# Performance work log

Hardware: AMD Instinct MI355X
Metric: run time of the kernel (lower is better)

Reference implementation:

```python
import jax, jax.numpy as jnp
import numpy as np

N_NODES = 100_000
N_EDGES = 1_600_000
IN_F = 256
HID = 256
OUT_F = 256
BN_EPS = 1e-5


def make_quaternion_mul(kernel):
    # kernel: [d, 4m] -> hamilton: [4d, 4m]
    dim = kernel.shape[1] // 4
    r, i, j, k = jnp.split(kernel, 4, axis=1)
    r2 = jnp.concatenate([r, -i, -j, -k], axis=0)
    i2 = jnp.concatenate([i, r, -k, j], axis=0)
    j2 = jnp.concatenate([j, k, r, -i], axis=0)
    k2 = jnp.concatenate([k, -j, i, r], axis=0)
    return jnp.concatenate([r2, i2, j2, k2], axis=1)


def setup_inputs() -> dict:
    key = jax.random.key(0)
    ks = jax.random.split(key, 6)
    x = jax.random.normal(ks[0], (N_NODES, IN_F), dtype=jnp.float32)
    rows = jax.random.randint(ks[1], (N_EDGES,), 0, N_NODES, dtype=jnp.int32)
    cols = jax.random.randint(ks[2], (N_EDGES,), 0, N_NODES, dtype=jnp.int32)
    edge_vals = jax.random.uniform(ks[3], (N_EDGES,), dtype=jnp.float32)
    stdv1 = np.sqrt(6.0 / (IN_F // 4 + HID))
    weight1 = jax.random.uniform(ks[4], (IN_F // 4, HID), dtype=jnp.float32,
                                 minval=-stdv1, maxval=stdv1)
    stdv2 = np.sqrt(6.0 / (HID // 4 + OUT_F))
    weight2 = jax.random.uniform(ks[5], (HID // 4, OUT_F), dtype=jnp.float32,
                                 minval=-stdv2, maxval=stdv2)
    gamma = jnp.ones((HID,), dtype=jnp.float32)
    beta = jnp.zeros((HID,), dtype=jnp.float32)
    return {"x": x, "rows": rows, "cols": cols, "edge_vals": edge_vals,
            "weight1": weight1, "weight2": weight2, "gamma": gamma, "beta": beta}


def reference(x, rows, cols, edge_vals, weight1, weight2, gamma, beta):
    hamilton1 = make_quaternion_mul(weight1)  # [IN_F, HID]
    hamilton2 = make_quaternion_mul(weight2)  # [HID, OUT_F]
    # spmm: new_x[r] = sum_e adj[r,c]*x[c] over edges (r=rows, c=cols)
    gathered = edge_vals[:, None] * x[cols]               # [E, IN_F]
    new_x = jax.ops.segment_sum(gathered, rows, num_segments=N_NODES)
    out1 = new_x @ hamilton1                              # [N, HID]
    # BatchNorm1d (training mode): biased batch stats over nodes
    mean = jnp.mean(out1, axis=0)
    var = jnp.mean(jnp.square(out1 - mean), axis=0)
    out1 = (out1 - mean) * jax.lax.rsqrt(var + BN_EPS) * gamma + beta
    out1 = jnp.tanh(out1)
    return out1 @ hamilton2                               # [N, OUT_F]
```

## Files before the change

kernel.cpp:

```cpp
#include <hip/hip_runtime.h>
#include <hip/hip_bf16.h>
#include <math.h>


#define FDIM 256
#define NREP 32
#define CH 2048

typedef __attribute__((ext_vector_type(8))) short bf16x8;
typedef __attribute__((ext_vector_type(4))) float f32x4;

static __device__ inline short f2bf(float x) {
    __hip_bfloat16 h = __float2bfloat16(x);
    return *reinterpret_cast<short*>(&h);
}
static __device__ inline float bf2f(unsigned short u) {
    union { unsigned int i; float f; } c;
    c.i = ((unsigned int)u) << 16;
    return c.f;
}
static __device__ inline float fast_tanh(float x) {
    float e = __expf(2.f * x);
    return 1.f - 2.f * __builtin_amdgcn_rcpf(e + 1.f);
}

static __device__ void build_hfrag(const float* __restrict__ w, ushort* __restrict__ hf,
                                   int t) {
    const int   comp_t[16] = {0,1,2,3,  1,0,3,2,  2,3,0,1,  3,2,1,0};
    const float sign_t[16] = {1,1,1,1, -1,1,1,-1, -1,-1,1,1, -1,1,-1,1};
    int f = t >> 6, lane = t & 63;
    int tile = f >> 3, kk = f & 7;
    int col = tile * 16 + (lane & 15);
    int b = col >> 6, q = col & 63;
    ushort o[8];
#pragma unroll
    for (int j = 0; j < 8; ++j) {
        int k = kk * 32 + ((lane >> 4) << 3) + j;
        int a = k >> 6, p = k & 63;
        int ab = a * 4 + b;
        float v = sign_t[ab] * w[p * 256 + comp_t[ab] * 64 + q];
        o[j] = (ushort)f2bf(v);
    }
    *(ushort4*)(hf + (size_t)t * 8)     = make_ushort4(o[0], o[1], o[2], o[3]);
    *(ushort4*)(hf + (size_t)t * 8 + 4) = make_ushort4(o[4], o[5], o[6], o[7]);
}

__global__ __launch_bounds__(256) void k_initp1(const float* __restrict__ w1,
                                                const float* __restrict__ w2,
                                                ushort* __restrict__ h1f,
                                                ushort* __restrict__ h2f,
                                                float* __restrict__ statsR,
                                                const int* __restrict__ rows,
                                                int* __restrict__ CM,
                                                int E, int nchunk, int NB) {
    int b = blockIdx.x;
    if (b < 32) {
        build_hfrag(w1, h1f, b * 256 + threadIdx.x);
        return;
    }
    if (b < 64) {
        build_hfrag(w2, h2f, (b - 32) * 256 + threadIdx.x);
        return;
    }
    if (b < 80) {
        int slot = (b - 64) * 256 + threadIdx.x;
        *(float4*)(statsR + slot * 4) = make_float4(0.f, 0.f, 0.f, 0.f);
        return;
    }
    __shared__ int lc[256];
    int t = threadIdx.x, c = b - 80;
    lc[t] = 0;
    __syncthreads();
#pragma unroll
    for (int i = 0; i < 8; ++i) {
        int e = c * CH + i * 256 + t;
        if (e < E) atomicAdd(&lc[rows[e] >> 9], 1);
    }
    __syncthreads();
    if (t < NB) CM[t * nchunk + c] = lc[t];
}

__global__ __launch_bounds__(256) void k_p2(const int* __restrict__ CM,
                                            int* __restrict__ PO,
                                            int* __restrict__ BT, int nchunk) {
    __shared__ int ts[256];
    int t = threadIdx.x, b = blockIdx.x;
    int base = b * nchunk;
    int lex[4], s = 0;
#pragma unroll
    for (int i = 0; i < 4; ++i) {
        int c = t * 4 + i;
        int v = (c < nchunk) ? CM[base + c] : 0;
        lex[i] = s;
        s += v;
    }
    ts[t] = s;
    __syncthreads();
    for (int off = 1; off < 256; off <<= 1) {
        int v = (t >= off) ? ts[t - off] : 0;
        __syncthreads();
        ts[t] += v;
        __syncthreads();
    }
    int excl = ts[t] - s;
#pragma unroll
    for (int i = 0; i < 4; ++i) {
        int c = t * 4 + i;
        if (c < nchunk) PO[base + c] = excl + lex[i];
    }
    if (t == 255) BT[b] = ts[255];
}

__global__ __launch_bounds__(256) void k_p3(const int* __restrict__ rows,
                                            const int* __restrict__ cols,
                                            const float* __restrict__ vals,
                                            const int* __restrict__ PO,
                                            const int* __restrict__ BT,
                                            uint2* __restrict__ tmp2,
                                            int E, int nchunk, int NB) {
    __shared__ int sBB[256];
    __shared__ int sPO[256];
    __shared__ int sLC[256];
    int t = threadIdx.x, c = blockIdx.x;
    int own = (t < NB) ? BT[t] : 0;
    sBB[t] = own;
    sPO[t] = (t < NB) ? PO[t * nchunk + c] : 0;
    sLC[t] = 0;
    __syncthreads();
    for (int off = 1; off < 256; off <<= 1) {
        int v = (t >= off) ? sBB[t - off] : 0;
        __syncthreads();
        sBB[t] += v;
        __syncthreads();
    }
    sBB[t] -= own;
    __syncthreads();
#pragma unroll
    for (int i = 0; i < 8; ++i) {
        int e = c * CH + i * 256 + t;
        if (e < E) {
            int r = rows[e];
            int b = r >> 9;
            int rank = atomicAdd(&sLC[b], 1);
            int pos = sBB[b] + sPO[b] + rank;
            int iv = (int)(vals[e] * 32768.0f);
            tmp2[pos] = make_uint2((unsigned int)cols[e] | ((unsigned int)iv << 17),
                                   (unsigned int)r);
        }
    }
}

__global__ __launch_bounds__(1024) void k_p4(const uint2* __restrict__ tmp2,
                                             const int* __restrict__ BT,
                                             unsigned int* __restrict__ ew,
                                             int* __restrict__ offs,
                                             int N, int NB) {
    __shared__ int sBB[256];
    __shared__ int sH[512];
    __shared__ int sO[512];
    __shared__ int sC[512];
    int t = threadIdx.x, b = blockIdx.x;
    int own = 0;
    if (t < 256) {
        own = (t < NB) ? BT[t] : 0;
        sBB[t] = own;
    }
    __syncthreads();
    for (int off = 1; off < 256; off <<= 1) {
        int v = (t < 256 && t >= off) ? sBB[t - off] : 0;
        __syncthreads();
        if (t < 256) sBB[t] += v;
        __syncthreads();
    }
    if (t < 256) sBB[t] -= own;
    if (t < 512) sH[t] = 0;
    __syncthreads();
    const int base = sBB[b];
    const int nE = BT[b];
    const int rbase = b << 9;
    for (int i = t; i < nE; i += 1024)
        atomicAdd(&sH[(int)tmp2[base + i].y - rbase], 1);
    __syncthreads();
    if (t < 512) sO[t] = sH[t];
    __syncthreads();
    for (int off = 1; off < 512; off <<= 1) {
        int v = (t < 512 && t >= off) ? sO[t - off] : 0;
        __syncthreads();
        if (t < 512) sO[t] += v;
        __syncthreads();
    }
    if (t < 512) {
        sO[t] -= sH[t];
        int r = rbase + t;
        if (r <= N) offs[r] = base + sO[t];
        sC[t] = 0;
    }
    __syncthreads();
    for (int i = t; i < nE; i += 1024) {
        uint2 u = tmp2[base + i];
        int lr = (int)u.y - rbase;
        int p = atomicAdd(&sC[lr], 1);
        ew[base + sO[lr] + p] = u.x;
    }
}

__global__ __launch_bounds__(256) void k_gemm1(const float* __restrict__ X,
                                               const ushort* __restrict__ Bf,
                                               ushort* __restrict__ Y, int N) {
    __shared__ ushort lds[16384];
    const int t = threadIdx.x;
    const int w = t >> 6, lane = t & 63;
    const int r0 = blockIdx.x * 128 + w * 32;
    const int kbase = ((lane >> 4) & 3) * 8;
    const int rA[2] = { min(r0 + (lane & 15), N - 1),
                        min(r0 + 16 + (lane & 15), N - 1) };

    bf16x8 af[2][8];
#pragma unroll
    for (int rt = 0; rt < 2; ++rt)
#pragma unroll
        for (int kk = 0; kk < 8; ++kk) {
            const float* p = X + (size_t)rA[rt] * 256 + kk * 32 + kbase;
            float4 v0 = *(const float4*)p;
            float4 v1 = *(const float4*)(p + 4);
            bf16x8 a;
            a[0] = f2bf(v0.x); a[1] = f2bf(v0.y); a[2] = f2bf(v0.z); a[3] = f2bf(v0.w);
            a[4] = f2bf(v1.x); a[5] = f2bf(v1.y); a[6] = f2bf(v1.z); a[7] = f2bf(v1.w);
            af[rt][kk] = a;
        }

    for (int g = 0; g < 4; ++g) {
        {
            const float4* s4 = (const float4*)(Bf + (size_t)g * 16384);
            float4* d4 = (float4*)lds;
#pragma unroll
            for (int i = 0; i < 8; ++i) d4[i * 256 + t] = s4[i * 256 + t];
        }
        __syncthreads();

        f32x4 acc[2][4];
#pragma unroll
        for (int rt = 0; rt < 2; ++rt)
#pragma unroll
            for (int tg = 0; tg < 4; ++tg) acc[rt][tg] = (f32x4){0.f, 0.f, 0.f, 0.f};

#pragma unroll
        for (int tg = 0; tg < 4; ++tg)
#pragma unroll
            for (int kk = 0; kk < 8; ++kk) {
                bf16x8 b = *(const bf16x8*)(lds + ((tg * 8 + kk) * 64 + lane) * 8);
                acc[0][tg] = __builtin_amdgcn_mfma_f32_16x16x32_bf16(af[0][kk], b, acc[0][tg], 0, 0, 0);
                acc[1][tg] = __builtin_amdgcn_mfma_f32_16x16x32_bf16(af[1][kk], b, acc[1][tg], 0, 0, 0);
            }

#pragma unroll
        for (int tg = 0; tg < 4; ++tg) {
            int col = (g * 4 + tg) * 16 + (lane & 15);
#pragma unroll
            for (int rt = 0; rt < 2; ++rt) {
                int rbase = r0 + rt * 16 + ((lane >> 4) & 3) * 4;
#pragma unroll
                for (int j = 0; j < 4; ++j) {
                    int r = rbase + j;
                    if (r < N) Y[(size_t)r * 256 + col] = (ushort)f2bf(acc[rt][tg][j]);
                }
            }
        }
        __syncthreads();
    }
}

__global__ __launch_bounds__(256) void k_spmm(const ushort* __restrict__ Y,
                                              const int* __restrict__ offs,
                                              const unsigned int* __restrict__ ew,
                                              ushort* __restrict__ O,
                                              float* __restrict__ statsR,
                                              int n, int W) {
    __shared__ float ls_s[4][256];
    __shared__ float ls_q[4][256];
    const int tid = threadIdx.x;
    const int w = tid >> 6, lane = tid & 63;
    const int gw = blockIdx.x * 4 + w;

    float s0 = 0.f, s1 = 0.f, s2 = 0.f, s3 = 0.f;
    float q0 = 0.f, q1 = 0.f, q2 = 0.f, q3 = 0.f;

    for (int k = 0; k < 4; ++k) {
        int row = gw + k * W;
        bool ok = row < n;
        int r = ok ? row : 0;
        int beg = offs[r];
        int cnt = ok ? offs[r + 1] - beg : 0;
        int g = (cnt + 7) >> 3;
        const unsigned int* ep = ew + beg;

        float a0 = 0.f, a1 = 0.f, a2 = 0.f, a3 = 0.f;
        unsigned int wv[8];
        if (g > 0) {
#pragma unroll
            for (int i = 0; i < 8; ++i) wv[i] = ep[i];
        }
        for (int gi = 0; gi < g; ++gi) {
            unsigned int wn[8];
            bool more = (gi + 1) < g;
            if (more) {
#pragma unroll
                for (int i = 0; i < 8; ++i) wn[i] = ep[(gi + 1) * 8 + i];
            }
#pragma unroll
            for (int i = 0; i < 8; ++i) {
                int idx = gi * 8 + i;
                unsigned int wd = wv[i];
                int c = (idx < cnt) ? (int)(wd & 0x1FFFFu) : 0;
                float v = (idx < cnt) ? (float)(wd >> 17) * (1.0f / 32768.0f) : 0.f;
                ushort4 yv = *(const ushort4*)(Y + (size_t)c * 256 + lane * 4);
                a0 = fmaf(v, bf2f(yv.x), a0);
                a1 = fmaf(v, bf2f(yv.y), a1);
                a2 = fmaf(v, bf2f(yv.z), a2);
                a3 = fmaf(v, bf2f(yv.w), a3);
            }
            if (more) {
#pragma unroll
                for (int i = 0; i < 8; ++i) wv[i] = wn[i];
            }
        }
        if (ok) {
            ushort4 o = make_ushort4((ushort)f2bf(a0), (ushort)f2bf(a1),
                                     (ushort)f2bf(a2), (ushort)f2bf(a3));
            *(ushort4*)(O + (size_t)r * 512 + lane * 4) = o;
        }
        s0 += a0; q0 = fmaf(a0, a0, q0);
        s1 += a1; q1 = fmaf(a1, a1, q1);
        s2 += a2; q2 = fmaf(a2, a2, q2);
        s3 += a3; q3 = fmaf(a3, a3, q3);
    }

    int rep = blockIdx.x & (NREP - 1);
    *(float4*)&ls_s[w][lane * 4] = make_float4(s0, s1, s2, s3);
    *(float4*)&ls_q[w][lane * 4] = make_float4(q0, q1, q2, q3);
    __syncthreads();
    float sv = ls_s[0][tid] + ls_s[1][tid] + ls_s[2][tid] + ls_s[3][tid];
    float qv = ls_q[0][tid] + ls_q[1][tid] + ls_q[2][tid] + ls_q[3][tid];
    atomicAdd(&statsR[rep * 256 + tid], sv);
    atomicAdd(&statsR[NREP * 256 + rep * 256 + tid], qv);
}

__global__ __launch_bounds__(256) void k_gemm2(void* __restrict__ Av,
                                               const ushort* __restrict__ Bf,
                                               const float* __restrict__ statsR,
                                               const float* __restrict__ gamma,
                                               const float* __restrict__ beta, int N) {
    __shared__ ushort lds[16384];
    __shared__ float sscl[256], sshf[256];
    const int t = threadIdx.x;
    const int w = t >> 6, lane = t & 63;
    const int r0 = blockIdx.x * 128 + w * 32;
    const int kbase = ((lane >> 4) & 3) * 8;
    const int rA[2] = { min(r0 + (lane & 15), N - 1),
                        min(r0 + 16 + (lane & 15), N - 1) };

    {
        float s = 0.f, q = 0.f;
#pragma unroll
        for (int i = 0; i < NREP; ++i) {
            s += statsR[i * 256 + t];
            q += statsR[NREP * 256 + i * 256 + t];
        }
        float invn = 1.0f / (float)N;
        float mean = s * invn;
        float var = q * invn - mean * mean;
        float inv = rsqrtf(var + 1e-5f);
        float gg = gamma[t] * inv;
        sscl[t] = gg;
        sshf[t] = beta[t] - mean * gg;
        __syncthreads();
    }

    const ushort* X = (const ushort*)Av;
    bf16x8 af[2][8];
#pragma unroll
    for (int rt = 0; rt < 2; ++rt)
#pragma unroll
        for (int kk = 0; kk < 8; ++kk) {
            const ushort* p = X + (size_t)rA[rt] * 512 + kk * 32 + kbase;
            ushort4 u0 = *(const ushort4*)p;
            ushort4 u1 = *(const ushort4*)(p + 4);
            float4 s0 = *(const float4*)&sscl[kk * 32 + kbase];
            float4 s1 = *(const float4*)&sscl[kk * 32 + kbase + 4];
            float4 h0 = *(const float4*)&sshf[kk * 32 + kbase];
            float4 h1 = *(const float4*)&sshf[kk * 32 + kbase + 4];
            bf16x8 a;
            a[0] = f2bf(fast_tanh(fmaf(bf2f(u0.x), s0.x, h0.x)));
            a[1] = f2bf(fast_tanh(fmaf(bf2f(u0.y), s0.y, h0.y)));
            a[2] = f2bf(fast_tanh(fmaf(bf2f(u0.z), s0.z, h0.z)));
            a[3] = f2bf(fast_tanh(fmaf(bf2f(u0.w), s0.w, h0.w)));
            a[4] = f2bf(fast_tanh(fmaf(bf2f(u1.x), s1.x, h1.x)));
            a[5] = f2bf(fast_tanh(fmaf(bf2f(u1.y), s1.y, h1.y)));
            a[6] = f2bf(fast_tanh(fmaf(bf2f(u1.z), s1.z, h1.z)));
            a[7] = f2bf(fast_tanh(fmaf(bf2f(u1.w), s1.w, h1.w)));
            af[rt][kk] = a;
        }

    float* Cf = (float*)Av;
    for (int g = 0; g < 4; ++g) {
        {
            const float4* s4 = (const float4*)(Bf + (size_t)g * 16384);
            float4* d4 = (float4*)lds;
#pragma unroll
            for (int i = 0; i < 8; ++i) d4[i * 256 + t] = s4[i * 256 + t];
        }
        __syncthreads();

        f32x4 acc[2][4];
#pragma unroll
        for (int rt = 0; rt < 2; ++rt)
#pragma unroll
            for (int tg = 0; tg < 4; ++tg) acc[rt][tg] = (f32x4){0.f, 0.f, 0.f, 0.f};

#pragma unroll
        for (int tg = 0; tg < 4; ++tg)
#pragma unroll
            for (int kk = 0; kk < 8; ++kk) {
                bf16x8 b = *(const bf16x8*)(lds + ((tg * 8 + kk) * 64 + lane) * 8);
                acc[0][tg] = __builtin_amdgcn_mfma_f32_16x16x32_bf16(af[0][kk], b, acc[0][tg], 0, 0, 0);
                acc[1][tg] = __builtin_amdgcn_mfma_f32_16x16x32_bf16(af[1][kk], b, acc[1][tg], 0, 0, 0);
            }

#pragma unroll
        for (int tg = 0; tg < 4; ++tg) {
            int col = (g * 4 + tg) * 16 + (lane & 15);
#pragma unroll
            for (int rt = 0; rt < 2; ++rt) {
                int rbase = r0 + rt * 16 + ((lane >> 4) & 3) * 4;
#pragma unroll
                for (int j = 0; j < 4; ++j) {
                    int r = rbase + j;
                    if (r < N) Cf[(size_t)r * 256 + col] = acc[rt][tg][j];
                }
            }
        }
        __syncthreads();
    }
}

extern "C" void kernel_launch(void* const* d_in, const int* in_sizes, int n_in,
                              void* d_out, int out_size, void* d_ws, size_t ws_size,
                              hipStream_t stream) {
    const float* x     = (const float*)d_in[0];
    const int* rows    = (const int*)d_in[1];
    const int* cols    = (const int*)d_in[2];
    const float* evin  = (const float*)d_in[3];
    const float* w1    = (const float*)d_in[4];
    const float* w2    = (const float*)d_in[5];
    const float* gamma = (const float*)d_in[6];
    const float* beta  = (const float*)d_in[7];
    float* out = (float*)d_out;

    const int N = in_sizes[0] / FDIM;
    const int E = in_sizes[1];
    const int NB = (N + 511) >> 9;
    const int nchunk = (E + CH - 1) / CH;

    char* ws = (char*)d_ws;
    size_t o = 0;
    auto alloc = [&](size_t bytes) -> char* {
        char* p = ws + o;
        o += (bytes + 255) & ~(size_t)255;
        return p;
    };
    ushort* h1f  = (ushort*)alloc(128 * 64 * 8 * 2);
    ushort* h2f  = (ushort*)alloc(128 * 64 * 8 * 2);
    ushort* y    = (ushort*)alloc((size_t)N * 256 * 2);
    float* statsR = (float*)alloc(2 * NREP * 256 * 4);
    int*   CM    = (int*)alloc((size_t)NB * nchunk * 4);
    int*   PO    = (int*)alloc((size_t)NB * nchunk * 4);
    int*   BT    = (int*)alloc(256 * 4);
    uint2* tmp2  = (uint2*)alloc((size_t)E * 8);
    unsigned int* ewp = (unsigned int*)alloc(((size_t)E + 16) * 4);
    int*   offs  = (int*)alloc((size_t)(N + 1) * 4);

    k_initp1<<<80 + nchunk, 256, 0, stream>>>(w1, w2, h1f, h2f, statsR,
                                              rows, CM, E, nchunk, NB);
    k_p2<<<NB, 256, 0, stream>>>(CM, PO, BT, nchunk);
    k_p3<<<nchunk, 256, 0, stream>>>(rows, cols, evin, PO, BT, tmp2, E, nchunk, NB);
    k_p4<<<NB, 1024, 0, stream>>>(tmp2, BT, ewp, offs, N, NB);

    int gblk = (N + 127) / 128;
    k_gemm1<<<gblk, 256, 0, stream>>>(x, h1f, y, N);
    int W = (N + 3) / 4;
    int sblk = (W + 3) / 4;
    k_spmm<<<sblk, 256, 0, stream>>>(y, offs, ewp, (ushort*)out, statsR, N, W);
    k_gemm2<<<gblk, 256, 0, stream>>>(out, h2f, statsR, gamma, beta, N);
}
```

Before: 267.6 us.

## Pad CSR rows to multiples of 8 and stage GEMM outputs through LDS

The CSR build now pads each row's edge list to a multiple of 8 with zero entries and stores (begin, padded count) pairs. This lets the SpMM inner loop drop its per-edge bounds checks. Padding entries decode to column 0 with weight 0, so they do extra gathers of row 0 that contribute nothing. Both GEMM kernels now write their output tiles into LDS first and then issue coalesced 16-byte row stores, replacing scattered 2- or 4-byte column-strided stores. This costs an extra barrier and LDS round trip per column group.

```diff
diff --git a/kernel.cpp b/kernel.cpp
--- a/kernel.cpp
+++ b/kernel.cpp
@@ -153,11 +153,12 @@
 __global__ __launch_bounds__(1024) void k_p4(const uint2* __restrict__ tmp2,
                                              const int* __restrict__ BT,
                                              unsigned int* __restrict__ ew,
-                                             int* __restrict__ offs,
+                                             uint2* __restrict__ offs2,
                                              int N, int NB) {
     __shared__ int sBB[256];
     __shared__ int sH[512];
-    __shared__ int sO[512];
+    __shared__ int sHp[512];
+    __shared__ int sOp[512];
     __shared__ int sC[512];
     int t = threadIdx.x, b = blockIdx.x;
     int own = 0;
@@ -176,23 +177,29 @@
     if (t < 512) sH[t] = 0;
     __syncthreads();
     const int base = sBB[b];
+    const int basePad = sBB[b] + b * 4096;
     const int nE = BT[b];
     const int rbase = b << 9;
     for (int i = t; i < nE; i += 1024)
         atomicAdd(&sH[(int)tmp2[base + i].y - rbase], 1);
     __syncthreads();
-    if (t < 512) sO[t] = sH[t];
+    if (t < 512) {
+        int hp = (sH[t] + 7) & ~7;
+        sHp[t] = hp;
+        sOp[t] = hp;
+    }
     __syncthreads();
     for (int off = 1; off < 512; off <<= 1) {
-        int v = (t < 512 && t >= off) ? sO[t - off] : 0;
-        __syncthreads();
-        if (t < 512) sO[t] += v;
+        int v = (t < 512 && t >= off) ? sOp[t - off] : 0;
+        __syncthreads();
+        if (t < 512) sOp[t] += v;
         __syncthreads();
     }
     if (t < 512) {
-        sO[t] -= sH[t];
+        sOp[t] -= sHp[t];
         int r = rbase + t;
-        if (r <= N) offs[r] = base + sO[t];
+        if (r < N) offs2[r] = make_uint2((unsigned int)(basePad + sOp[t]),
+                                         (unsigned int)sHp[t]);
         sC[t] = 0;
     }
     __syncthreads();
@@ -200,20 +207,26 @@
         uint2 u = tmp2[base + i];
         int lr = (int)u.y - rbase;
         int p = atomicAdd(&sC[lr], 1);
-        ew[base + sO[lr] + p] = u.x;
+        ew[basePad + sOp[lr] + p] = u.x;
+    }
+    if (t < 512) {
+        int e0 = basePad + sOp[t] + sH[t];
+        int e1 = basePad + sOp[t] + sHp[t];
+        for (int e = e0; e < e1; ++e) ew[e] = 0u;
     }
 }
 
 __global__ __launch_bounds__(256) void k_gemm1(const float* __restrict__ X,
                                                const ushort* __restrict__ Bf,
                                                ushort* __restrict__ Y, int N) {
-    __shared__ ushort lds[16384];
+    __shared__ float4 lds4[2048];
+    ushort* lds = (ushort*)lds4;
     const int t = threadIdx.x;
     const int w = t >> 6, lane = t & 63;
     const int r0 = blockIdx.x * 128 + w * 32;
-    const int kbase = ((lane >> 4) & 3) * 8;
-    const int rA[2] = { min(r0 + (lane & 15), N - 1),
-                        min(r0 + 16 + (lane & 15), N - 1) };
+    const int q = (lane >> 4) & 3, l = lane & 15;
+    const int kbase = q * 8;
+    const int rA[2] = { min(r0 + l, N - 1), min(r0 + 16 + l, N - 1) };
 
     bf16x8 af[2][8];
 #pragma unroll
@@ -232,9 +245,8 @@
     for (int g = 0; g < 4; ++g) {
         {
             const float4* s4 = (const float4*)(Bf + (size_t)g * 16384);
-            float4* d4 = (float4*)lds;
-#pragma unroll
-            for (int i = 0; i < 8; ++i) d4[i * 256 + t] = s4[i * 256 + t];
+#pragma unroll
+            for (int i = 0; i < 8; ++i) lds4[i * 256 + t] = s4[i * 256 + t];
         }
         __syncthreads();
 
@@ -252,18 +264,25 @@
                 acc[0][tg] = __builtin_amdgcn_mfma_f32_16x16x32_bf16(af[0][kk], b, acc[0][tg], 0, 0, 0);
                 acc[1][tg] = __builtin_amdgcn_mfma_f32_16x16x32_bf16(af[1][kk], b, acc[1][tg], 0, 0, 0);
             }
-
-#pragma unroll
-        for (int tg = 0; tg < 4; ++tg) {
-            int col = (g * 4 + tg) * 16 + (lane & 15);
-#pragma unroll
-            for (int rt = 0; rt < 2; ++rt) {
-                int rbase = r0 + rt * 16 + ((lane >> 4) & 3) * 4;
-#pragma unroll
-                for (int j = 0; j < 4; ++j) {
-                    int r = rbase + j;
-                    if (r < N) Y[(size_t)r * 256 + col] = (ushort)f2bf(acc[rt][tg][j]);
-                }
+        __syncthreads();
+
+        {
+            ushort* cw = lds + w * 2048;
+#pragma unroll
+            for (int tg = 0; tg < 4; ++tg)
+#pragma unroll
+                for (int rt = 0; rt < 2; ++rt)
+#pragma unroll
+                    for (int j = 0; j < 4; ++j)
+                        cw[(rt * 16 + q * 4 + j) * 64 + tg * 16 + l] =
+                            (ushort)f2bf(acc[rt][tg][j]);
+            int gcol0 = g * 64;
+#pragma unroll
+            for (int p = 0; p < 4; ++p) {
+                uint4 rd = *(const uint4*)(lds + w * 2048 + p * 512 + lane * 8);
+                int row = r0 + p * 8 + (lane >> 3);
+                int col = gcol0 + (lane & 7) * 8;
+                if (row < N) *(uint4*)(Y + (size_t)row * 256 + col) = rd;
             }
         }
         __syncthreads();
@@ -271,7 +290,7 @@
 }
 
 __global__ __launch_bounds__(256) void k_spmm(const ushort* __restrict__ Y,
-                                              const int* __restrict__ offs,
+                                              const uint2* __restrict__ offs2,
                                               const unsigned int* __restrict__ ew,
                                               ushort* __restrict__ O,
                                               float* __restrict__ statsR,
@@ -289,10 +308,10 @@
         int row = gw + k * W;
         bool ok = row < n;
         int r = ok ? row : 0;
-        int beg = offs[r];
-        int cnt = ok ? offs[r + 1] - beg : 0;
-        int g = (cnt + 7) >> 3;
-        const unsigned int* ep = ew + beg;
+        uint2 bc = offs2[r];
+        int cnt = ok ? (int)bc.y : 0;
+        int g = cnt >> 3;
+        const unsigned int* ep = ew + bc.x;
 
         float a0 = 0.f, a1 = 0.f, a2 = 0.f, a3 = 0.f;
         unsigned int wv[8];
@@ -309,10 +328,9 @@
             }
 #pragma unroll
             for (int i = 0; i < 8; ++i) {
-                int idx = gi * 8 + i;
                 unsigned int wd = wv[i];
-                int c = (idx < cnt) ? (int)(wd & 0x1FFFFu) : 0;
-                float v = (idx < cnt) ? (float)(wd >> 17) * (1.0f / 32768.0f) : 0.f;
+                int c = (int)(wd & 0x1FFFFu);
+                float v = (float)(wd >> 17) * (1.0f / 32768.0f);
                 ushort4 yv = *(const ushort4*)(Y + (size_t)c * 256 + lane * 4);
                 a0 = fmaf(v, bf2f(yv.x), a0);
                 a1 = fmaf(v, bf2f(yv.y), a1);
@@ -350,25 +368,26 @@
                                                const float* __restrict__ statsR,
                                                const float* __restrict__ gamma,
                                                const float* __restrict__ beta, int N) {
-    __shared__ ushort lds[16384];
+    __shared__ float4 lds4[2048];
+    ushort* lds = (ushort*)lds4;
     __shared__ float sscl[256], sshf[256];
     const int t = threadIdx.x;
     const int w = t >> 6, lane = t & 63;
     const int r0 = blockIdx.x * 128 + w * 32;
-    const int kbase = ((lane >> 4) & 3) * 8;
-    const int rA[2] = { min(r0 + (lane & 15), N - 1),
-                        min(r0 + 16 + (lane & 15), N - 1) };
+    const int q = (lane >> 4) & 3, l = lane & 15;
+    const int kbase = q * 8;
+    const int rA[2] = { min(r0 + l, N - 1), min(r0 + 16 + l, N - 1) };
 
     {
-        float s = 0.f, q = 0.f;
+        float s = 0.f, qq = 0.f;
 #pragma unroll
         for (int i = 0; i < NREP; ++i) {
             s += statsR[i * 256 + t];
-            q += statsR[NREP * 256 + i * 256 + t];
+            qq += statsR[NREP * 256 + i * 256 + t];
         }
         float invn = 1.0f / (float)N;
         float mean = s * invn;
-        float var = q * invn - mean * mean;
+        float var = qq * invn - mean * mean;
         float inv = rsqrtf(var + 1e-5f);
         float gg = gamma[t] * inv;
         sscl[t] = gg;
@@ -405,9 +424,8 @@
     for (int g = 0; g < 4; ++g) {
         {
             const float4* s4 = (const float4*)(Bf + (size_t)g * 16384);
-            float4* d4 = (float4*)lds;
-#pragma unroll
-            for (int i = 0; i < 8; ++i) d4[i * 256 + t] = s4[i * 256 + t];
+#pragma unroll
+            for (int i = 0; i < 8; ++i) lds4[i * 256 + t] = s4[i * 256 + t];
         }
         __syncthreads();
 
@@ -425,18 +443,24 @@
                 acc[0][tg] = __builtin_amdgcn_mfma_f32_16x16x32_bf16(af[0][kk], b, acc[0][tg], 0, 0, 0);
                 acc[1][tg] = __builtin_amdgcn_mfma_f32_16x16x32_bf16(af[1][kk], b, acc[1][tg], 0, 0, 0);
             }
-
-#pragma unroll
-        for (int tg = 0; tg < 4; ++tg) {
-            int col = (g * 4 + tg) * 16 + (lane & 15);
-#pragma unroll
-            for (int rt = 0; rt < 2; ++rt) {
-                int rbase = r0 + rt * 16 + ((lane >> 4) & 3) * 4;
-#pragma unroll
-                for (int j = 0; j < 4; ++j) {
-                    int r = rbase + j;
-                    if (r < N) Cf[(size_t)r * 256 + col] = acc[rt][tg][j];
-                }
+        __syncthreads();
+
+        {
+            float* cw = (float*)lds4 + w * 2048;
+#pragma unroll
+            for (int tg = 0; tg < 4; ++tg)
+#pragma unroll
+                for (int rt = 0; rt < 2; ++rt)
+#pragma unroll
+                    for (int j = 0; j < 4; ++j)
+                        cw[(rt * 16 + q * 4 + j) * 64 + tg * 16 + l] = acc[rt][tg][j];
+            int gcol0 = g * 64;
+#pragma unroll
+            for (int p = 0; p < 8; ++p) {
+                float4 rd = *(const float4*)((float*)lds4 + w * 2048 + p * 256 + lane * 4);
+                int row = r0 + p * 4 + (lane >> 4);
+                int col = gcol0 + (lane & 15) * 4;
+                if (row < N) *(float4*)(Cf + (size_t)row * 256 + col) = rd;
             }
         }
         __syncthreads();
@@ -476,19 +500,19 @@
     int*   PO    = (int*)alloc((size_t)NB * nchunk * 4);
     int*   BT    = (int*)alloc(256 * 4);
     uint2* tmp2  = (uint2*)alloc((size_t)E * 8);
-    unsigned int* ewp = (unsigned int*)alloc(((size_t)E + 16) * 4);
-    int*   offs  = (int*)alloc((size_t)(N + 1) * 4);
+    unsigned int* ewp = (unsigned int*)alloc(((size_t)E + (size_t)NB * 4096 + 16) * 4);
+    uint2* offs2 = (uint2*)alloc((size_t)N * 8);
 
     k_initp1<<<80 + nchunk, 256, 0, stream>>>(w1, w2, h1f, h2f, statsR,
                                               rows, CM, E, nchunk, NB);
     k_p2<<<NB, 256, 0, stream>>>(CM, PO, BT, nchunk);
     k_p3<<<nchunk, 256, 0, stream>>>(rows, cols, evin, PO, BT, tmp2, E, nchunk, NB);
-    k_p4<<<NB, 1024, 0, stream>>>(tmp2, BT, ewp, offs, N, NB);
+    k_p4<<<NB, 1024, 0, stream>>>(tmp2, BT, ewp, offs2, N, NB);
 
     int gblk = (N + 127) / 128;
     k_gemm1<<<gblk, 256, 0, stream>>>(x, h1f, y, N);
     int W = (N + 3) / 4;
     int sblk = (W + 3) / 4;
-    k_spmm<<<sblk, 256, 0, stream>>>(y, offs, ewp, (ushort*)out, statsR, N, W);
+    k_spmm<<<sblk, 256, 0, stream>>>(y, offs2, ewp, (ushort*)out, statsR, N, W);
     k_gemm2<<<gblk, 256, 0, stream>>>(out, h2f, statsR, gamma, beta, N);
 }
```

Result: faster. 256.8 us (-4.0%).
